# Kernel optimization log

Hardware: AMD Instinct MI355X
Metric: run time of the kernel (lower is better)

Reference implementation:

```python
import jax, jax.numpy as jnp
import numpy as np

B, T, E, H, QKV = 4, 2048, 1024, 16, 64
D = E // H  # head_dim = 64


def setup_inputs() -> dict:
    key = jax.random.key(0)
    k1, k2, k3, k4 = jax.random.split(key, 4)
    scale = 1.0 / np.sqrt(D)
    x = jax.random.normal(k1, (B, T, E), dtype=jnp.float32)
    W_q = jax.random.normal(k2, (QKV, D), dtype=jnp.float32) * scale
    W_k = jax.random.normal(k3, (QKV, D), dtype=jnp.float32) * scale
    W_v = jax.random.normal(k4, (QKV, D), dtype=jnp.float32) * scale
    return {"x": x, "W_q": W_q, "W_k": W_k, "W_v": W_v}


def reference(x, W_q, W_k, W_v):
    Bx, Tx, Ex = x.shape
    d = Ex // H
    # [B,T,E] -> [B,H,T,D]  (same as torch view + permute(0,2,1,3))
    xh = x.reshape(Bx, Tx, H, d).transpose(0, 2, 1, 3)
    # Shared per-head projections: Linear(d -> qkv_dim), weight stored [out,in]
    Q = jnp.einsum("bhtd,qd->bhtq", xh, W_q)
    K = jnp.einsum("bhtd,qd->bhtq", xh, W_k)
    V = jnp.einsum("bhtd,qd->bhtq", xh, W_v)
    # NOTE: original scales by head_dim**0.5, not qkv_dim**0.5
    scores = jnp.einsum("bhtq,bhsq->bhts", Q, K) / jnp.asarray(d, x.dtype) ** 0.5
    attn = jax.nn.softmax(scores, axis=-1)
    out = jnp.einsum("bhts,bhsq->bhtq", attn, V) + V  # attention + V residual
    # per-head concat on last dim == head-major merge: [B,H,T,Q] -> [B,T,H*Q]
    return out.transpose(0, 2, 1, 3).reshape(Bx, Tx, H * W_q.shape[0])
```

## Files before the change

### kernel.cpp

```cpp
#include <hip/hip_runtime.h>

#define T_SEQ 2048
#define N_B   4
#define N_H   16
#define D_H   64
#define EMB   1024
#define CSC   0.18033688011f

typedef __attribute__((ext_vector_type(8))) short vshort8;
typedef __attribute__((ext_vector_type(4))) float vfloat4;

__device__ __forceinline__ ushort f2bf(float f) {
  union { float f; unsigned u; } v; v.f = f;
  unsigned u = v.u;
  return (ushort)((u + 0x7fffu + ((u >> 16) & 1u)) >> 16);
}
__device__ __forceinline__ unsigned pk2bf(float a, float b) {
  return (unsigned)f2bf(a) | ((unsigned)f2bf(b) << 16);
}
__device__ __forceinline__ float bf2f(ushort b) {
  union { unsigned u; float f; } v; v.u = ((unsigned)b) << 16;
  return v.f;
}
__device__ __forceinline__ float fexp2(float x) {
#if __has_builtin(__builtin_amdgcn_exp2f)
  return __builtin_amdgcn_exp2f(x);
#else
  return exp2f(x);
#endif
}
__device__ __forceinline__ unsigned permhi(float hi, float lo) {
  union { float f; unsigned u; } a, b; a.f = hi; b.f = lo;
#if __has_builtin(__builtin_amdgcn_perm)
  return __builtin_amdgcn_perm(a.u, b.u, 0x07060302u);
#else
  return (a.u & 0xFFFF0000u) | (b.u >> 16);
#endif
}
__device__ __forceinline__ vshort8 cvt8(const float* p) {
  float4 w0 = *(const float4*)(p);
  float4 w1 = *(const float4*)(p + 4);
  vshort8 t;
  t[0] = (short)f2bf(w0.x); t[1] = (short)f2bf(w0.y);
  t[2] = (short)f2bf(w0.z); t[3] = (short)f2bf(w0.w);
  t[4] = (short)f2bf(w1.x); t[5] = (short)f2bf(w1.y);
  t[6] = (short)f2bf(w1.z); t[7] = (short)f2bf(w1.w);
  return t;
}


__global__ void wconv(const float* __restrict__ Wq, const float* __restrict__ Wk,
                      const float* __restrict__ Wv, ushort* __restrict__ Wb) {
  const int lane = threadIdx.x & 63;
  const int l15  = lane & 15;
  const int quad = lane >> 4;
  const float* Ws[3] = {Wq, Wk, Wv};
#pragma unroll
  for (int m = 0; m < 3; ++m)
#pragma unroll
    for (int kc = 0; kc < 2; ++kc)
#pragma unroll
      for (int nt = 0; nt < 4; ++nt) {
        vshort8 t = cvt8(Ws[m] + (nt * 16 + l15) * D_H + kc * 32 + quad * 8);
        *(vshort8*)(&Wb[(((m * 2 + kc) * 4 + nt) * 64 + lane) * 8]) = t;
      }
}

__global__ __launch_bounds__(256, 4) void proj_qkv(
    const float* __restrict__ x, const ushort* __restrict__ Wb,
    uint2* __restrict__ Qb, uint2* __restrict__ Kb, uint2* __restrict__ Vb) {
  const int wid  = threadIdx.x >> 6;
  const int lane = threadIdx.x & 63;
  const int l15  = lane & 15;
  const int quad = lane >> 4;
  const int gw    = blockIdx.x * 4 + wid;
  const int strip = gw >> 4;
  const int h     = gw & 15;
  const int r0    = strip * 16;
  const int b     = r0 >> 11;
  const int bh    = b * N_H + h;
  const int ts    = (r0 & (T_SEQ - 1)) >> 4;

  vshort8 afr[2];
  {
    const float* xp = x + (size_t)(r0 + l15) * EMB + h * D_H + quad * 8;
    afr[0] = cvt8(xp);
    afr[1] = cvt8(xp + 32);
  }

  uint2* Bs[3] = {Qb, Kb, Vb};
#pragma unroll
  for (int m = 0; m < 3; ++m) {
    vshort8 wf[2][4];
#pragma unroll
    for (int kc = 0; kc < 2; ++kc)
#pragma unroll
      for (int nt = 0; nt < 4; ++nt)
        wf[kc][nt] = *(const vshort8*)(&Wb[(((m * 2 + kc) * 4 + nt) * 64 + lane) * 8]);
    vfloat4 acc[4];
#pragma unroll
    for (int nt = 0; nt < 4; ++nt) acc[nt] = (vfloat4){0.f, 0.f, 0.f, 0.f};
#pragma unroll
    for (int kc = 0; kc < 2; ++kc)
#pragma unroll
      for (int nt = 0; nt < 4; ++nt)
        acc[nt] = (m < 2)
          ? __builtin_amdgcn_mfma_f32_16x16x32_bf16(wf[kc][nt], afr[kc], acc[nt], 0, 0, 0)
          : __builtin_amdgcn_mfma_f32_16x16x32_bf16(afr[kc], wf[kc][nt], acc[nt], 0, 0, 0);
    uint2* B = Bs[m];
#pragma unroll
    for (int nt = 0; nt < 4; ++nt) {
      vfloat4 a = acc[nt];
      if (m == 0) { a[0] *= CSC; a[1] *= CSC; a[2] *= CSC; a[3] *= CSC; }
      uint2 w;
      w.x = pk2bf(a[0], a[1]);
      w.y = pk2bf(a[2], a[3]);
      B[(((size_t)bh * 128 + ts) * 4 + nt) * 64 + l15 * 4 + quad] = w;
    }
  }
}

__global__ __launch_bounds__(256, 3) void attn_fused(
    const uint2* __restrict__ Qb, const uint2* __restrict__ Kb,
    const uint2* __restrict__ Vb, float* __restrict__ out) {
  __shared__ ushort Pa[4 * 1024];

  const int tid  = threadIdx.x;
  const int wid  = tid >> 6;
  const int lane = tid & 63;
  const int l15  = lane & 15;
  const int quad = lane >> 4;
  const int qh   = quad >> 1;
  const int q1   = quad & 1;

  const int blk  = blockIdx.x;
  const int work = (blk & 7) * 128 + (blk >> 3);
  const int bh   = work >> 4;
  const int tblk = work & 15;
  const int b = bh >> 4, h = bh & 15;
  const int tstrip0 = tblk * 8 + wid * 2;

  const size_t hb = (size_t)bh * 128;
  const int laneoff = l15 * 4 + 2 * q1;

  vshort8 qf[2][2];
#pragma unroll
  for (int st = 0; st < 2; ++st)
#pragma unroll
    for (int kc = 0; kc < 2; ++kc)
      qf[st][kc] = *(const vshort8*)(&Qb[((hb + tstrip0 + st) * 4 + 2 * kc + qh) * 64 + laneoff]);

  vfloat4 oacc[2][4];
  float lsum[2];
#pragma unroll
  for (int st = 0; st < 2; ++st) {
#pragma unroll
    for (int nt = 0; nt < 4; ++nt) oacc[st][nt] = (vfloat4){0.f, 0.f, 0.f, 0.f};
    lsum[st] = 0.f;
  }

  ushort* Paw = &Pa[wid * 1024];
  const int parow = l15 * 64;
  const int swz   = l15 & 7;

  for (int ss = 0; ss < 128; ss += 4) {
    vshort8 kf[4][2];
#pragma unroll
    for (int snt = 0; snt < 4; ++snt)
#pragma unroll
      for (int kc = 0; kc < 2; ++kc)
        kf[snt][kc] = *(const vshort8*)(&Kb[((hb + ss + snt) * 4 + 2 * kc + qh) * 64 + laneoff]);
    vshort8 vf[2][4];
#pragma unroll
    for (int kc2 = 0; kc2 < 2; ++kc2)
#pragma unroll
      for (int dnt = 0; dnt < 4; ++dnt)
        vf[kc2][dnt] = *(const vshort8*)(&Vb[((hb + ss + 2 * kc2 + qh) * 4 + dnt) * 64 + laneoff]);

#pragma unroll
    for (int st = 0; st < 2; ++st) {
      vfloat4 sacc[4];
#pragma unroll
      for (int nt = 0; nt < 4; ++nt) sacc[nt] = (vfloat4){0.f, 0.f, 0.f, 0.f};
#pragma unroll
      for (int kc = 0; kc < 2; ++kc)
#pragma unroll
        for (int nt = 0; nt < 4; ++nt)
          sacc[nt] = __builtin_amdgcn_mfma_f32_16x16x32_bf16(kf[nt][kc], qf[st][kc], sacc[nt], 0, 0, 0);

      float ls = 0.f;
#pragma unroll
      for (int nt = 0; nt < 4; ++nt) {
        const float p0 = fexp2(sacc[nt][0]);
        const float p1 = fexp2(sacc[nt][1]);
        const float p2 = fexp2(sacc[nt][2]);
        const float p3 = fexp2(sacc[nt][3]);
        ls += (p0 + p1) + (p2 + p3);
        uint2 w;
        w.x = permhi(p1, p0);
        w.y = permhi(p3, p2);
        *(uint2*)(&Paw[parow + (((2 * nt + qh) ^ swz) << 3) + 4 * q1]) = w;
      }
      lsum[st] += ls;

#pragma unroll
      for (int kc2 = 0; kc2 < 2; ++kc2) {
        vshort8 pf = *(const vshort8*)(&Paw[parow + (((4 * kc2 + quad) ^ swz) << 3)]);
#pragma unroll
        for (int dnt = 0; dnt < 4; ++dnt)
          oacc[st][dnt] = __builtin_amdgcn_mfma_f32_16x16x32_bf16(pf, vf[kc2][dnt], oacc[st][dnt], 0, 0, 0);
      }
    }
  }

#pragma unroll
  for (int st = 0; st < 2; ++st) {
    float l = lsum[st];
    l += __shfl_xor(l, 16, 64);
    l += __shfl_xor(l, 32, 64);
    const float inv = 1.0f / l;
    float iT[4];
#pragma unroll
    for (int r = 0; r < 4; ++r) iT[r] = __shfl(inv, quad * 4 + r, 64);
    const int tstrip = tstrip0 + st;
#pragma unroll
    for (int nt = 0; nt < 4; ++nt) {
      uint2 vr = Vb[((hb + tstrip) * 4 + nt) * 64 + l15 * 4 + quad];
      float vres[4];
      vres[0] = bf2f((ushort)(vr.x & 0xFFFFu));
      vres[1] = bf2f((ushort)(vr.x >> 16));
      vres[2] = bf2f((ushort)(vr.y & 0xFFFFu));
      vres[3] = bf2f((ushort)(vr.y >> 16));
#pragma unroll
      for (int r = 0; r < 4; ++r) {
        const int t = tstrip * 16 + quad * 4 + r;
        out[((size_t)(b * T_SEQ + t)) * EMB + h * D_H + nt * 16 + l15] =
            oacc[st][nt][r] * iT[r] + vres[r];
      }
    }
  }
}

extern "C" void kernel_launch(void* const* d_in, const int* in_sizes, int n_in,
                              void* d_out, int out_size, void* d_ws, size_t ws_size,
                              hipStream_t stream) {
  const float* x  = (const float*)d_in[0];
  const float* Wq = (const float*)d_in[1];
  const float* Wk = (const float*)d_in[2];
  const float* Wv = (const float*)d_in[3];
  float* out = (float*)d_out;

  const size_t per = (size_t)64 * 128 * 4 * 16 * 4;
  uint2* Qb = (uint2*)d_ws;
  uint2* Kb = Qb + per;
  uint2* Vb = Kb + per;
  ushort* Wb = (ushort*)(Vb + per);

  wconv<<<1, 64, 0, stream>>>(Wq, Wk, Wv, Wb);
  proj_qkv<<<2048, 256, 0, stream>>>(x, Wb, Qb, Kb, Vb);
  attn_fused<<<1024, 256, 0, stream>>>(Qb, Kb, Vb, out);
}
```

Baseline: 190.3 us.

## Switch attention to 32x32x16 MFMA with register-shuffled P and new QKV layout

Rewrites the attention kernel to use 32x32x16 bf16 MFMA tiles instead of 16x16x32, so each wave handles 64 query rows against 64-key chunks per iteration. The P matrix is passed from the score accumulator into the PV MFMA operand through lane-xor shuffles, which removes the LDS staging buffer and its writes and reads. The projection kernel writes Q/K/V in a new tiled layout that matches the 32-row fragments. Block count halves and launch bounds drop to 2 waves per SIMD, which trades occupancy for higher register use and fewer operand reloads.

Measured after the change: 172.9 us. 9.1% less time.

```diff
diff --git a/kernel.cpp b/kernel.cpp
--- a/kernel.cpp
+++ b/kernel.cpp
@@ -7,8 +7,9 @@
 #define EMB   1024
 #define CSC   0.18033688011f
 
-typedef __attribute__((ext_vector_type(8))) short vshort8;
-typedef __attribute__((ext_vector_type(4))) float vfloat4;
+typedef __attribute__((ext_vector_type(8))) short   vshort8;
+typedef __attribute__((ext_vector_type(4))) float   vfloat4;
+typedef __attribute__((ext_vector_type(16))) float  vfloat16;
 
 __device__ __forceinline__ ushort f2bf(float f) {
   union { float f; unsigned u; } v; v.f = f;
@@ -72,18 +73,18 @@
   const int wid  = threadIdx.x >> 6;
   const int lane = threadIdx.x & 63;
   const int l15  = lane & 15;
-  const int quad = lane >> 4;
+  const int q    = lane >> 4;
   const int gw    = blockIdx.x * 4 + wid;
   const int strip = gw >> 4;
-  const int h     = gw & 15;
+  const int hd    = gw & 15;
   const int r0    = strip * 16;
   const int b     = r0 >> 11;
-  const int bh    = b * N_H + h;
+  const int bh    = b * N_H + hd;
   const int ts    = (r0 & (T_SEQ - 1)) >> 4;
 
   vshort8 afr[2];
   {
-    const float* xp = x + (size_t)(r0 + l15) * EMB + h * D_H + quad * 8;
+    const float* xp = x + (size_t)(r0 + l15) * EMB + hd * D_H + q * 8;
     afr[0] = cvt8(xp);
     afr[1] = cvt8(xp + 32);
   }
@@ -115,127 +116,141 @@
       uint2 w;
       w.x = pk2bf(a[0], a[1]);
       w.y = pk2bf(a[2], a[3]);
-      B[(((size_t)bh * 128 + ts) * 4 + nt) * 64 + l15 * 4 + quad] = w;
+      size_t idx;
+      if (m < 2) {
+        idx = ((size_t)(bh * 64 + (ts >> 1)) * 4 + nt) * 128
+              + (l15 + 16 * (ts & 1)) * 4 + q;
+      } else {
+        idx = (((size_t)(bh * 32 + (ts >> 2)) * 4 + (ts & 3)) * 2 + (nt >> 1)) * 128
+              + 64 * (nt & 1) + l15 * 4 + q;
+      }
+      B[idx] = w;
     }
   }
 }
 
-__global__ __launch_bounds__(256, 3) void attn_fused(
-    const uint2* __restrict__ Qb, const uint2* __restrict__ Kb,
-    const uint2* __restrict__ Vb, float* __restrict__ out) {
-  __shared__ ushort Pa[4 * 1024];
-
+__global__ __launch_bounds__(256, 2) void attn_fused(
+    const uint4* __restrict__ Qb, const uint4* __restrict__ Kb,
+    const uint4* __restrict__ Vb, float* __restrict__ out) {
   const int tid  = threadIdx.x;
   const int wid  = tid >> 6;
   const int lane = tid & 63;
-  const int l15  = lane & 15;
-  const int quad = lane >> 4;
-  const int qh   = quad >> 1;
-  const int q1   = quad & 1;
+  const int l31  = lane & 31;
+  const int h    = lane >> 5;
 
   const int blk  = blockIdx.x;
-  const int work = (blk & 7) * 128 + (blk >> 3);
-  const int bh   = work >> 4;
-  const int tblk = work & 15;
-  const int b = bh >> 4, h = bh & 15;
-  const int tstrip0 = tblk * 8 + wid * 2;
-
-  const size_t hb = (size_t)bh * 128;
-  const int laneoff = l15 * 4 + 2 * q1;
-
-  vshort8 qf[2][2];
-#pragma unroll
-  for (int st = 0; st < 2; ++st)
-#pragma unroll
-    for (int kc = 0; kc < 2; ++kc)
-      qf[st][kc] = *(const vshort8*)(&Qb[((hb + tstrip0 + st) * 4 + 2 * kc + qh) * 64 + laneoff]);
-
-  vfloat4 oacc[2][4];
-  float lsum[2];
-#pragma unroll
-  for (int st = 0; st < 2; ++st) {
-#pragma unroll
-    for (int nt = 0; nt < 4; ++nt) oacc[st][nt] = (vfloat4){0.f, 0.f, 0.f, 0.f};
-    lsum[st] = 0.f;
-  }
-
-  ushort* Paw = &Pa[wid * 1024];
-  const int parow = l15 * 64;
-  const int swz   = l15 & 7;
-
-  for (int ss = 0; ss < 128; ss += 4) {
-    vshort8 kf[4][2];
-#pragma unroll
-    for (int snt = 0; snt < 4; ++snt)
-#pragma unroll
-      for (int kc = 0; kc < 2; ++kc)
-        kf[snt][kc] = *(const vshort8*)(&Kb[((hb + ss + snt) * 4 + 2 * kc + qh) * 64 + laneoff]);
-    vshort8 vf[2][4];
-#pragma unroll
-    for (int kc2 = 0; kc2 < 2; ++kc2)
-#pragma unroll
-      for (int dnt = 0; dnt < 4; ++dnt)
-        vf[kc2][dnt] = *(const vshort8*)(&Vb[((hb + ss + 2 * kc2 + qh) * 4 + dnt) * 64 + laneoff]);
-
-#pragma unroll
-    for (int st = 0; st < 2; ++st) {
-      vfloat4 sacc[4];
-#pragma unroll
-      for (int nt = 0; nt < 4; ++nt) sacc[nt] = (vfloat4){0.f, 0.f, 0.f, 0.f};
-#pragma unroll
-      for (int kc = 0; kc < 2; ++kc)
-#pragma unroll
-        for (int nt = 0; nt < 4; ++nt)
-          sacc[nt] = __builtin_amdgcn_mfma_f32_16x16x32_bf16(kf[nt][kc], qf[st][kc], sacc[nt], 0, 0, 0);
-
+  const int work = (blk & 7) * 64 + (blk >> 3);
+  const int bh   = work >> 3;
+  const int tblk8 = work & 7;
+  const int b = bh >> 4, hh = bh & 15;
+  const int T64 = tblk8 * 4 + wid;
+
+  const int lo = l31 * 2 + h;
+
+  vshort8 qf[2][4];
+#pragma unroll
+  for (int tb = 0; tb < 2; ++tb)
+#pragma unroll
+    for (int ds = 0; ds < 4; ++ds)
+      qf[tb][ds] = *(const vshort8*)&Qb[((size_t)(bh * 64 + 2 * T64 + tb) * 4 + ds) * 64 + lo];
+
+  vfloat16 oacc[2][2];
+#pragma unroll
+  for (int tb = 0; tb < 2; ++tb)
+#pragma unroll
+    for (int db = 0; db < 2; ++db)
+#pragma unroll
+      for (int i = 0; i < 16; ++i) oacc[tb][db][i] = 0.f;
+  float lsum[2] = {0.f, 0.f};
+
+#pragma unroll 1
+  for (int ss = 0; ss < 32; ++ss) {
+    vshort8 kf[2][4];
+#pragma unroll
+    for (int sb = 0; sb < 2; ++sb)
+#pragma unroll
+      for (int ds = 0; ds < 4; ++ds)
+        kf[sb][ds] = *(const vshort8*)&Kb[((size_t)(bh * 64 + 2 * ss + sb) * 4 + ds) * 64 + lo];
+    vshort8 vf[4][2];
+#pragma unroll
+    for (int st = 0; st < 4; ++st)
+#pragma unroll
+      for (int db = 0; db < 2; ++db)
+        vf[st][db] = *(const vshort8*)&Vb[(((size_t)(bh * 32 + ss) * 4 + st) * 2 + db) * 64 + lo];
+
+#pragma unroll
+    for (int tb = 0; tb < 2; ++tb) {
+      vfloat16 sacc[2];
+#pragma unroll
+      for (int sb = 0; sb < 2; ++sb) {
+#pragma unroll
+        for (int i = 0; i < 16; ++i) sacc[sb][i] = 0.f;
+#pragma unroll
+        for (int ds = 0; ds < 4; ++ds)
+          sacc[sb] = __builtin_amdgcn_mfma_f32_32x32x16_bf16(kf[sb][ds], qf[tb][ds], sacc[sb], 0, 0, 0);
+      }
+      float p[2][16];
       float ls = 0.f;
 #pragma unroll
-      for (int nt = 0; nt < 4; ++nt) {
-        const float p0 = fexp2(sacc[nt][0]);
-        const float p1 = fexp2(sacc[nt][1]);
-        const float p2 = fexp2(sacc[nt][2]);
-        const float p3 = fexp2(sacc[nt][3]);
-        ls += (p0 + p1) + (p2 + p3);
-        uint2 w;
-        w.x = permhi(p1, p0);
-        w.y = permhi(p3, p2);
-        *(uint2*)(&Paw[parow + (((2 * nt + qh) ^ swz) << 3) + 4 * q1]) = w;
-      }
-      lsum[st] += ls;
-
-#pragma unroll
-      for (int kc2 = 0; kc2 < 2; ++kc2) {
-        vshort8 pf = *(const vshort8*)(&Paw[parow + (((4 * kc2 + quad) ^ swz) << 3)]);
-#pragma unroll
-        for (int dnt = 0; dnt < 4; ++dnt)
-          oacc[st][dnt] = __builtin_amdgcn_mfma_f32_16x16x32_bf16(pf, vf[kc2][dnt], oacc[st][dnt], 0, 0, 0);
-      }
+      for (int sb = 0; sb < 2; ++sb)
+#pragma unroll
+        for (int r = 0; r < 16; ++r) {
+          p[sb][r] = fexp2(sacc[sb][r]);
+          ls += p[sb][r];
+        }
+      lsum[tb] += ls;
+
+#pragma unroll
+      for (int sb = 0; sb < 2; ++sb)
+#pragma unroll
+        for (int g = 0; g < 2; ++g) {
+          const unsigned OL0 = permhi(p[sb][8 * g + 1], p[sb][8 * g + 0]);
+          const unsigned OL1 = permhi(p[sb][8 * g + 3], p[sb][8 * g + 2]);
+          const unsigned OH0 = permhi(p[sb][8 * g + 5], p[sb][8 * g + 4]);
+          const unsigned OH1 = permhi(p[sb][8 * g + 7], p[sb][8 * g + 6]);
+          const unsigned s0 = h ? OL0 : OH0;
+          const unsigned s1 = h ? OL1 : OH1;
+          const unsigned r0 = (unsigned)__shfl_xor((int)s0, 32, 64);
+          const unsigned r1 = (unsigned)__shfl_xor((int)s1, 32, 64);
+          union { unsigned u[4]; vshort8 v; } pa;
+          pa.u[0] = h ? r0 : OL0;
+          pa.u[1] = h ? r1 : OL1;
+          pa.u[2] = h ? OH0 : r0;
+          pa.u[3] = h ? OH1 : r1;
+          const int st = 2 * sb + g;
+#pragma unroll
+          for (int db = 0; db < 2; ++db)
+            oacc[tb][db] = __builtin_amdgcn_mfma_f32_32x32x16_bf16(pa.v, vf[st][db], oacc[tb][db], 0, 0, 0);
+        }
     }
   }
 
-#pragma unroll
-  for (int st = 0; st < 2; ++st) {
-    float l = lsum[st];
-    l += __shfl_xor(l, 16, 64);
-    l += __shfl_xor(l, 32, 64);
+  const uint2* Vb2 = (const uint2*)Vb;
+#pragma unroll
+  for (int tb = 0; tb < 2; ++tb) {
+    const float l = lsum[tb] + __shfl_xor(lsum[tb], 32, 64);
     const float inv = 1.0f / l;
-    float iT[4];
-#pragma unroll
-    for (int r = 0; r < 4; ++r) iT[r] = __shfl(inv, quad * 4 + r, 64);
-    const int tstrip = tstrip0 + st;
-#pragma unroll
-    for (int nt = 0; nt < 4; ++nt) {
-      uint2 vr = Vb[((hb + tstrip) * 4 + nt) * 64 + l15 * 4 + quad];
-      float vres[4];
-      vres[0] = bf2f((ushort)(vr.x & 0xFFFFu));
-      vres[1] = bf2f((ushort)(vr.x >> 16));
-      vres[2] = bf2f((ushort)(vr.y & 0xFFFFu));
-      vres[3] = bf2f((ushort)(vr.y >> 16));
-#pragma unroll
-      for (int r = 0; r < 4; ++r) {
-        const int t = tstrip * 16 + quad * 4 + r;
-        out[((size_t)(b * T_SEQ + t)) * EMB + h * D_H + nt * 16 + l15] =
-            oacc[st][nt][r] * iT[r] + vres[r];
+    const int T32 = 2 * T64 + tb;
+#pragma unroll
+    for (int db = 0; db < 2; ++db) {
+#pragma unroll
+      for (int rq = 0; rq < 4; ++rq) {
+        const int sq = 8 * T32 + 2 * rq + h;
+        uint2 vr = Vb2[(((size_t)(bh * 32 + (sq >> 4)) * 4 + ((sq >> 2) & 3)) * 2 + db) * 128
+                       + l31 * 4 + ((sq >> 1) & 1) * 2 + (sq & 1)];
+        float vres[4];
+        vres[0] = bf2f((ushort)(vr.x & 0xFFFFu));
+        vres[1] = bf2f((ushort)(vr.x >> 16));
+        vres[2] = bf2f((ushort)(vr.y & 0xFFFFu));
+        vres[3] = bf2f((ushort)(vr.y >> 16));
+#pragma unroll
+        for (int rr = 0; rr < 4; ++rr) {
+          const int row = rr + 8 * rq + 4 * h;
+          const float iT = __shfl(inv, row, 64);
+          const int t = T32 * 32 + row;
+          out[((size_t)(b * T_SEQ + t)) * EMB + hh * D_H + db * 32 + l31] =
+              oacc[tb][db][rq * 4 + rr] * iT + vres[rr];
+        }
       }
     }
   }
@@ -250,13 +265,13 @@
   const float* Wv = (const float*)d_in[3];
   float* out = (float*)d_out;
 
-  const size_t per = (size_t)64 * 128 * 4 * 16 * 4;
-  uint2* Qb = (uint2*)d_ws;
-  uint2* Kb = Qb + per;
-  uint2* Vb = Kb + per;
-  ushort* Wb = (ushort*)(Vb + per);
+  const size_t per4 = (size_t)64 * 64 * 4 * 64;
+  uint4* Qb = (uint4*)d_ws;
+  uint4* Kb = Qb + per4;
+  uint4* Vb = Kb + per4;
+  ushort* Wb = (ushort*)(Vb + per4);
 
   wconv<<<1, 64, 0, stream>>>(Wq, Wk, Wv, Wb);
-  proj_qkv<<<2048, 256, 0, stream>>>(x, Wb, Qb, Kb, Vb);
-  attn_fused<<<1024, 256, 0, stream>>>(Qb, Kb, Vb, out);
-}
+  proj_qkv<<<2048, 256, 0, stream>>>(x, Wb, (uint2*)Qb, (uint2*)Kb, (uint2*)Vb);
+  attn_fused<<<512, 256, 0, stream>>>(Qb, Kb, Vb, out);
+}
```
